# Performance work log

Measured on AMD Instinct MI355X. Metric: run time of the kernel, lower is better.

## Reference

```python
import jax, jax.numpy as jnp
import numpy as np

N_NODES = 100000
N_EDGES = 1600000
D_FEAT = 64
D_OUT = 64
K_HOPS = 2


def setup_inputs() -> dict:
    key = jax.random.key(0)
    k1, k2, k3, k4, k5 = jax.random.split(key, 5)
    feat = jax.random.normal(k1, (N_NODES, D_FEAT), dtype=jnp.float32)
    src = jax.random.randint(k2, (N_EDGES,), 0, N_NODES, dtype=jnp.int32)
    dst = jax.random.randint(k3, (N_EDGES,), 0, N_NODES, dtype=jnp.int32)
    # xavier-ish scale for fc1
    W1 = jax.random.normal(k4, (D_OUT, D_FEAT), dtype=jnp.float32) * (1.0 / np.sqrt(D_FEAT))
    b1 = jnp.zeros((D_OUT,), dtype=jnp.float32)
    return {"feat": feat, "src": src, "dst": dst, "W1": W1, "b1": b1}


def reference(feat, src, dst, W1, b1):
    # in-degrees (edges point src -> dst), clamp(min=1)
    deg = jax.ops.segment_sum(jnp.ones_like(dst, dtype=feat.dtype), dst,
                              num_segments=N_NODES)
    norm = jnp.power(jnp.maximum(deg, 1.0), -0.5)[:, None]  # [N, 1]
    # k hops of symmetric-normalized aggregation: h = D^-1/2 A D^-1/2 h
    for _ in range(K_HOPS):
        feat = feat * norm
        feat = jax.ops.segment_sum(feat[src], dst, num_segments=N_NODES)
        feat = feat * norm
    # fc1: x @ W1.T + b1
    return feat @ W1.T + b1
```

## Files before the change

kernel.cpp:

```cpp
#include <hip/hip_runtime.h>

#define NN 100000
#define NE 1600000
#define D 64
#define BSHIFT 7
#define NPB 128
#define NBUCK ((NN + NPB - 1) / NPB)
#define NCHUNK 512
#define CE (NE / NCHUNK)
#define CAP 4096
#define EBL 2560
#define NFC 1563

typedef unsigned int uint32;
typedef __attribute__((ext_vector_type(8))) short bf16x8;
typedef __attribute__((ext_vector_type(4))) float f32x4;

__device__ __forceinline__ uint32 f2bf(float f) {
    union { float f; uint32 i; } c; c.f = f;
    return (c.i + 0x7FFFu + ((c.i >> 16) & 1u)) >> 16;
}

__device__ __forceinline__ bf16x8 cvt8(const float* p) {
    float4 lo = *reinterpret_cast<const float4*>(p);
    float4 hi = *reinterpret_cast<const float4*>(p + 4);
    bf16x8 r;
    r[0] = (short)f2bf(lo.x); r[1] = (short)f2bf(lo.y);
    r[2] = (short)f2bf(lo.z); r[3] = (short)f2bf(lo.w);
    r[4] = (short)f2bf(hi.x); r[5] = (short)f2bf(hi.y);
    r[6] = (short)f2bf(hi.z); r[7] = (short)f2bf(hi.w);
    return r;
}

__global__ __launch_bounds__(256) void prep_part_kernel(const float* __restrict__ feat,
                                                        const float* __restrict__ W1,
                                                        unsigned short* __restrict__ fb,
                                                        const int* __restrict__ src,
                                                        const int* __restrict__ dst,
                                                        int* __restrict__ gcur,
                                                        int* __restrict__ ebuf) {
    __shared__ int ebl[CE];
    __shared__ unsigned short bkt[CE];
    __shared__ int cnt[NBUCK];
    __shared__ int bas[NBUCK];
    const int bid = blockIdx.x;
    if (bid >= NCHUNK) {
        const int wid = threadIdx.x >> 6;
        const int lane = threadIdx.x & 63;
        const int tile = (bid - NCHUNK) * 4 + wid;
        if (tile >= 6250) return;
        const int node0 = tile * 16;
        const int m = lane & 15;
        const int kg = lane >> 4;
        const float* frow = feat + (size_t)(node0 + m) * D + kg * 8;
        bf16x8 aF0 = cvt8(frow);
        bf16x8 aF1 = cvt8(frow + 32);
#pragma unroll
        for (int t = 0; t < 4; ++t) {
            const float* wrow = W1 + (size_t)(t * 16 + m) * D + kg * 8;
            bf16x8 bF0 = cvt8(wrow);
            bf16x8 bF1 = cvt8(wrow + 32);
            f32x4 acc = {0.f, 0.f, 0.f, 0.f};
            acc = __builtin_amdgcn_mfma_f32_16x16x32_bf16(aF0, bF0, acc, 0, 0, 0);
            acc = __builtin_amdgcn_mfma_f32_16x16x32_bf16(aF1, bF1, acc, 0, 0, 0);
            const int col = t * 16 + m;
#pragma unroll
            for (int r = 0; r < 4; ++r)
                fb[(size_t)(node0 + kg * 4 + r) * D + col] = (unsigned short)f2bf(acc[r]);
        }
        return;
    }
    for (int i = threadIdx.x; i < NBUCK; i += 256) cnt[i] = 0;
    __syncthreads();
    const int e0 = bid * CE;
    for (int i = threadIdx.x; i < CE; i += 256) {
        int d = dst[e0 + i], s = src[e0 + i];
        int b = d >> BSHIFT;
        ebl[i] = (s << BSHIFT) | (d & (NPB - 1));
        bkt[i] = (unsigned short)b;
        atomicAdd(&cnt[b], 1);
    }
    __syncthreads();
    for (int i = threadIdx.x; i < NBUCK; i += 256) {
        int c = cnt[i];
        bas[i] = c ? atomicAdd(&gcur[i], c) : 0;
    }
    __syncthreads();
    for (int i = threadIdx.x; i < NBUCK; i += 256) cnt[i] = 0;
    __syncthreads();
    for (int i = threadIdx.x; i < CE; i += 256) {
        int b = bkt[i];
        int p = bas[b] + atomicAdd(&cnt[b], 1);
        ebuf[(size_t)b * CAP + p] = ebl[i];
    }
}

__global__ __launch_bounds__(256) void bucketize_kernel(int* __restrict__ ebuf,
                                                        const int* __restrict__ gcur,
                                                        uint32* __restrict__ rpd,
                                                        float* __restrict__ norm) {
    __shared__ int ebl[EBL];
    __shared__ int cnt[NPB];
    __shared__ int sc[NPB + 1];
    __shared__ int lcur[NPB];
    const int b = blockIdx.x;
    const int base = b << BSHIFT;
    const int t = threadIdx.x;
    const int r0 = b * CAP;
    int len = gcur[b];
    if (len > EBL) len = EBL;
    if (t < NPB) { cnt[t] = 0; lcur[t] = 0; }
    if (t == 0) sc[0] = 0;
    __syncthreads();
    for (int e = t; e < len; e += 256) {
        int v = ebuf[r0 + e];
        ebl[e] = v;
        atomicAdd(&cnt[v & (NPB - 1)], 1);
    }
    __syncthreads();
    if (t < NPB) sc[t + 1] = cnt[t];
    __syncthreads();
    for (int off = 1; off < NPB; off <<= 1) {
        int v = (t < NPB && t >= off) ? sc[t + 1 - off] : 0;
        __syncthreads();
        if (t < NPB) sc[t + 1] += v;
        __syncthreads();
    }
    const int nval = min(NPB, NN - base);
    if (t < nval) {
        rpd[base + t] = ((uint32)(r0 + sc[t]) << 9) | (uint32)min(cnt[t], 511);
        norm[base + t] = rsqrtf(fmaxf((float)cnt[t], 1.0f));
    }
    __syncthreads();
    for (int e = t; e < len; e += 256) {
        int v = ebl[e];
        int ld = v & (NPB - 1);
        int p = r0 + sc[ld] + atomicAdd(&lcur[ld], 1);
        ebuf[p] = v & ~(NPB - 1);
    }
}

#define ACC8(Rr)                                 \
    a0 += __uint_as_float((Rr).x << 16);         \
    a1 += __uint_as_float((Rr).x & 0xFFFF0000u); \
    a2 += __uint_as_float((Rr).y << 16);         \
    a3 += __uint_as_float((Rr).y & 0xFFFF0000u); \
    a4 += __uint_as_float((Rr).z << 16);         \
    a5 += __uint_as_float((Rr).z & 0xFFFF0000u); \
    a6 += __uint_as_float((Rr).w << 16);         \
    a7 += __uint_as_float((Rr).w & 0xFFFF0000u);

#define ACC8W(Rr, W)                                   \
    a0 += (W) * __uint_as_float((Rr).x << 16);         \
    a1 += (W) * __uint_as_float((Rr).x & 0xFFFF0000u); \
    a2 += (W) * __uint_as_float((Rr).y << 16);         \
    a3 += (W) * __uint_as_float((Rr).y & 0xFFFF0000u); \
    a4 += (W) * __uint_as_float((Rr).z << 16);         \
    a5 += (W) * __uint_as_float((Rr).z & 0xFFFF0000u); \
    a6 += (W) * __uint_as_float((Rr).w << 16);         \
    a7 += (W) * __uint_as_float((Rr).w & 0xFFFF0000u);

#define STEP1(E)                                                           \
    {                                                                      \
        int o_ = csr[(E) + slot];                                          \
        uint4 r_ = *reinterpret_cast<const uint4*>(base + o_ + lo16);      \
        if constexpr (HOP == 1) { float w_ = norm[o_ >> 7]; ACC8W(r_, w_) } \
        else { ACC8(r_) }                                                  \
    }

template <int HOP>
__global__ __launch_bounds__(256) void gather_kernel(const unsigned short* __restrict__ in,
                                                     const uint32* __restrict__ rpd,
                                                     const int* __restrict__ csr,
                                                     const float* __restrict__ norm,
                                                     unsigned short* __restrict__ outb,
                                                     float* __restrict__ outf,
                                                     const float* __restrict__ b1) {
    const int node = blockIdx.x * 4 + (threadIdx.x >> 6);
    const int lane = threadIdx.x & 63;
    const int slot = lane >> 3;
    const int fo = (lane & 7) * 8;
    const int lo16 = (lane & 7) * 16;
    const char* base = (const char*)in;
    const uint32 v = rpd[node];
    int e = (int)(v >> 9);
    const int e1 = e + (int)(v & 511u);
    float a0 = 0, a1 = 0, a2 = 0, a3 = 0, a4 = 0, a5 = 0, a6 = 0, a7 = 0;
    for (; e + 16 <= e1; e += 16) {
        STEP1(e)
        STEP1(e + 8)
    }
    for (; e + 8 <= e1; e += 8) STEP1(e)
    if (e + slot < e1) STEP1(e)
#pragma unroll
    for (int off = 8; off <= 32; off <<= 1) {
        a0 += __shfl_xor(a0, off); a1 += __shfl_xor(a1, off);
        a2 += __shfl_xor(a2, off); a3 += __shfl_xor(a3, off);
        a4 += __shfl_xor(a4, off); a5 += __shfl_xor(a5, off);
        a6 += __shfl_xor(a6, off); a7 += __shfl_xor(a7, off);
    }
    if (slot == 0) {
        const float nd = norm[node];
        if (HOP == 1) {
            const float sc = nd * nd;
            uint4 o;
            o.x = f2bf(a0 * sc) | (f2bf(a1 * sc) << 16);
            o.y = f2bf(a2 * sc) | (f2bf(a3 * sc) << 16);
            o.z = f2bf(a4 * sc) | (f2bf(a5 * sc) << 16);
            o.w = f2bf(a6 * sc) | (f2bf(a7 * sc) << 16);
            *reinterpret_cast<uint4*>(outb + (size_t)node * D + fo) = o;
        } else {
            float4 bb = *reinterpret_cast<const float4*>(b1 + fo);
            float4 bc = *reinterpret_cast<const float4*>(b1 + fo + 4);
            float4 o1 = {a0 * nd + bb.x, a1 * nd + bb.y, a2 * nd + bb.z, a3 * nd + bb.w};
            float4 o2 = {a4 * nd + bc.x, a5 * nd + bc.y, a6 * nd + bc.z, a7 * nd + bc.w};
            float* op = outf + (size_t)node * D + fo;
            *reinterpret_cast<float4*>(op) = o1;
            *reinterpret_cast<float4*>(op + 4) = o2;
        }
    }
}

extern "C" void kernel_launch(void* const* d_in, const int* in_sizes, int n_in,
                              void* d_out, int out_size, void* d_ws, size_t ws_size,
                              hipStream_t stream) {
    const float* feat = (const float*)d_in[0];
    const int* src    = (const int*)d_in[1];
    const int* dst    = (const int*)d_in[2];
    const float* W1   = (const float*)d_in[3];
    const float* b1   = (const float*)d_in[4];
    float* out        = (float*)d_out;

    uint32*         rpd  = (uint32*)d_ws;
    float*          norm = (float*)(rpd + NN);
    int*            gcur = (int*)(norm + NN);
    int*            csr  = gcur + 1024;
    unsigned short* t1b  = (unsigned short*)(csr + (size_t)NBUCK * CAP);
    unsigned short* fb   = (unsigned short*)d_out;

    hipMemsetAsync(gcur, 0, NBUCK * sizeof(int), stream);
    prep_part_kernel<<<NCHUNK + NFC, 256, 0, stream>>>(feat, W1, fb, src, dst, gcur, csr);
    bucketize_kernel<<<NBUCK, 256, 0, stream>>>(csr, gcur, rpd, norm);

    gather_kernel<1><<<NN / 4, 256, 0, stream>>>(fb, rpd, csr, norm, t1b, nullptr, nullptr);
    gather_kernel<2><<<NN / 4, 256, 0, stream>>>(t1b, rpd, csr, norm, nullptr, out, b1);
}
```

Before: 144.0 us.

## Replace global atomic bucket offsets with per-chunk prefix tables and local partitioning

Each edge chunk now scans its own bucket counts and writes the edges locally sorted by bucket within its chunk slice, plus a per-chunk offset table. This removes the global atomicAdd on bucket cursors and the memset. The bucketize kernel reads each chunk's segment for its bucket via a prefix over chunks and builds the CSR in a separate buffer with a smaller per-bucket capacity. In exchange it reads 512 small scattered segments per bucket with a serial per-thread copy loop, and it aliases t1b onto ebuf.

```diff
diff --git a/kernel.cpp b/kernel.cpp
--- a/kernel.cpp
+++ b/kernel.cpp
@@ -8,8 +8,8 @@
 #define NBUCK ((NN + NPB - 1) / NPB)
 #define NCHUNK 512
 #define CE (NE / NCHUNK)
-#define CAP 4096
-#define EBL 2560
+#define BSTR (NBUCK + 1)
+#define CAPC 2560
 #define NFC 1563
 
 typedef unsigned int uint32;
@@ -32,21 +32,23 @@
     return r;
 }
 
-__global__ __launch_bounds__(256) void prep_part_kernel(const float* __restrict__ feat,
-                                                        const float* __restrict__ W1,
-                                                        unsigned short* __restrict__ fb,
-                                                        const int* __restrict__ src,
-                                                        const int* __restrict__ dst,
-                                                        int* __restrict__ gcur,
-                                                        int* __restrict__ ebuf) {
+__global__ __launch_bounds__(256) void build_kernel(const float* __restrict__ feat,
+                                                    const float* __restrict__ W1,
+                                                    unsigned short* __restrict__ fb,
+                                                    const int* __restrict__ src,
+                                                    const int* __restrict__ dst,
+                                                    int* __restrict__ basG,
+                                                    int* __restrict__ ebuf) {
     __shared__ int ebl[CE];
     __shared__ unsigned short bkt[CE];
     __shared__ int cnt[NBUCK];
-    __shared__ int bas[NBUCK];
+    __shared__ int sc[NBUCK + 1];
+    __shared__ int tsum[256];
     const int bid = blockIdx.x;
+    const int t = threadIdx.x;
     if (bid >= NCHUNK) {
-        const int wid = threadIdx.x >> 6;
-        const int lane = threadIdx.x & 63;
+        const int wid = t >> 6;
+        const int lane = t & 63;
         const int tile = (bid - NCHUNK) * 4 + wid;
         if (tile >= 6250) return;
         const int node0 = tile * 16;
@@ -56,24 +58,24 @@
         bf16x8 aF0 = cvt8(frow);
         bf16x8 aF1 = cvt8(frow + 32);
 #pragma unroll
-        for (int t = 0; t < 4; ++t) {
-            const float* wrow = W1 + (size_t)(t * 16 + m) * D + kg * 8;
+        for (int tt = 0; tt < 4; ++tt) {
+            const float* wrow = W1 + (size_t)(tt * 16 + m) * D + kg * 8;
             bf16x8 bF0 = cvt8(wrow);
             bf16x8 bF1 = cvt8(wrow + 32);
             f32x4 acc = {0.f, 0.f, 0.f, 0.f};
             acc = __builtin_amdgcn_mfma_f32_16x16x32_bf16(aF0, bF0, acc, 0, 0, 0);
             acc = __builtin_amdgcn_mfma_f32_16x16x32_bf16(aF1, bF1, acc, 0, 0, 0);
-            const int col = t * 16 + m;
+            const int col = tt * 16 + m;
 #pragma unroll
             for (int r = 0; r < 4; ++r)
                 fb[(size_t)(node0 + kg * 4 + r) * D + col] = (unsigned short)f2bf(acc[r]);
         }
         return;
     }
-    for (int i = threadIdx.x; i < NBUCK; i += 256) cnt[i] = 0;
+    for (int i = t; i < NBUCK; i += 256) cnt[i] = 0;
     __syncthreads();
     const int e0 = bid * CE;
-    for (int i = threadIdx.x; i < CE; i += 256) {
+    for (int i = t; i < CE; i += 256) {
         int d = dst[e0 + i], s = src[e0 + i];
         int b = d >> BSHIFT;
         ebl[i] = (s << BSHIFT) | (d & (NPB - 1));
@@ -81,62 +83,112 @@
         atomicAdd(&cnt[b], 1);
     }
     __syncthreads();
-    for (int i = threadIdx.x; i < NBUCK; i += 256) {
-        int c = cnt[i];
-        bas[i] = c ? atomicAdd(&gcur[i], c) : 0;
-    }
-    __syncthreads();
-    for (int i = threadIdx.x; i < NBUCK; i += 256) cnt[i] = 0;
-    __syncthreads();
-    for (int i = threadIdx.x; i < CE; i += 256) {
+    const int j0 = t * 4;
+    int v0 = (j0 + 0 < NBUCK) ? cnt[j0 + 0] : 0;
+    int v1 = (j0 + 1 < NBUCK) ? cnt[j0 + 1] : 0;
+    int v2 = (j0 + 2 < NBUCK) ? cnt[j0 + 2] : 0;
+    int v3 = (j0 + 3 < NBUCK) ? cnt[j0 + 3] : 0;
+    int s0 = v0, s1 = s0 + v1, s2 = s1 + v2, s3 = s2 + v3;
+    tsum[t] = s3;
+    __syncthreads();
+    for (int off = 1; off < 256; off <<= 1) {
+        int y = (t >= off) ? tsum[t - off] : 0;
+        __syncthreads();
+        tsum[t] += y;
+        __syncthreads();
+    }
+    const int pre = (t > 0) ? tsum[t - 1] : 0;
+    if (j0 + 0 < NBUCK) sc[j0 + 0] = pre;
+    if (j0 + 1 < NBUCK) sc[j0 + 1] = pre + s0;
+    if (j0 + 2 < NBUCK) sc[j0 + 2] = pre + s1;
+    if (j0 + 3 < NBUCK) sc[j0 + 3] = pre + s2;
+    if (t == 0) sc[NBUCK] = CE;
+    __syncthreads();
+    int* brow = basG + (size_t)bid * BSTR;
+    for (int j = t; j < BSTR; j += 256) brow[j] = sc[j];
+    for (int i = t; i < NBUCK; i += 256) cnt[i] = 0;
+    __syncthreads();
+    for (int i = t; i < CE; i += 256) {
         int b = bkt[i];
-        int p = bas[b] + atomicAdd(&cnt[b], 1);
-        ebuf[(size_t)b * CAP + p] = ebl[i];
-    }
-}
-
-__global__ __launch_bounds__(256) void bucketize_kernel(int* __restrict__ ebuf,
-                                                        const int* __restrict__ gcur,
+        int p = sc[b] + atomicAdd(&cnt[b], 1);
+        ebuf[e0 + p] = ebl[i];
+    }
+}
+
+__global__ __launch_bounds__(256) void bucketize_kernel(const int* __restrict__ ebuf,
+                                                        const int* __restrict__ basG,
+                                                        int* __restrict__ csr,
                                                         uint32* __restrict__ rpd,
                                                         float* __restrict__ norm) {
-    __shared__ int ebl[EBL];
+    __shared__ int stage[CAPC];
+    __shared__ int clo[NCHUNK];
+    __shared__ int clen[NCHUNK];
+    __shared__ int cpre[NCHUNK + 1];
+    __shared__ int tsum[256];
     __shared__ int cnt[NPB];
-    __shared__ int sc[NPB + 1];
+    __shared__ int sc2[NPB + 1];
     __shared__ int lcur[NPB];
     const int b = blockIdx.x;
     const int base = b << BSHIFT;
     const int t = threadIdx.x;
-    const int r0 = b * CAP;
-    int len = gcur[b];
-    if (len > EBL) len = EBL;
+    for (int c = t; c < NCHUNK; c += 256) {
+        int lo = basG[(size_t)c * BSTR + b];
+        int hi = basG[(size_t)c * BSTR + b + 1];
+        clo[c] = lo;
+        clen[c] = hi - lo;
+    }
     if (t < NPB) { cnt[t] = 0; lcur[t] = 0; }
-    if (t == 0) sc[0] = 0;
-    __syncthreads();
-    for (int e = t; e < len; e += 256) {
-        int v = ebuf[r0 + e];
-        ebl[e] = v;
-        atomicAdd(&cnt[v & (NPB - 1)], 1);
-    }
-    __syncthreads();
-    if (t < NPB) sc[t + 1] = cnt[t];
+    if (t == 0) sc2[0] = 0;
+    __syncthreads();
+    const int c0 = t * 2;
+    int w0 = clen[c0], w1 = clen[c0 + 1];
+    int u0 = w0, u1 = u0 + w1;
+    tsum[t] = u1;
+    __syncthreads();
+    for (int off = 1; off < 256; off <<= 1) {
+        int y = (t >= off) ? tsum[t - off] : 0;
+        __syncthreads();
+        tsum[t] += y;
+        __syncthreads();
+    }
+    const int pre = (t > 0) ? tsum[t - 1] : 0;
+    cpre[c0] = pre;
+    cpre[c0 + 1] = pre + u0;
+    if (t == 255) cpre[NCHUNK] = tsum[255];
+    __syncthreads();
+    int total = cpre[NCHUNK];
+    if (total > CAPC) total = CAPC;
+    for (int c = t; c < NCHUNK; c += 256) {
+        int lo = clo[c];
+        int n = clen[c];
+        int p = cpre[c];
+        if (p + n > CAPC) n = (p < CAPC) ? (CAPC - p) : 0;
+        const int* seg = ebuf + (size_t)c * CE + lo;
+        for (int k = 0; k < n; ++k) stage[p + k] = seg[k];
+    }
+    __syncthreads();
+    for (int e = t; e < total; e += 256)
+        atomicAdd(&cnt[stage[e] & (NPB - 1)], 1);
+    __syncthreads();
+    if (t < NPB) sc2[t + 1] = cnt[t];
     __syncthreads();
     for (int off = 1; off < NPB; off <<= 1) {
-        int v = (t < NPB && t >= off) ? sc[t + 1 - off] : 0;
-        __syncthreads();
-        if (t < NPB) sc[t + 1] += v;
+        int v = (t < NPB && t >= off) ? sc2[t + 1 - off] : 0;
+        __syncthreads();
+        if (t < NPB) sc2[t + 1] += v;
         __syncthreads();
     }
     const int nval = min(NPB, NN - base);
     if (t < nval) {
-        rpd[base + t] = ((uint32)(r0 + sc[t]) << 9) | (uint32)min(cnt[t], 511);
+        rpd[base + t] = ((uint32)(b * CAPC + sc2[t]) << 9) | (uint32)min(cnt[t], 511);
         norm[base + t] = rsqrtf(fmaxf((float)cnt[t], 1.0f));
     }
     __syncthreads();
-    for (int e = t; e < len; e += 256) {
-        int v = ebl[e];
+    for (int e = t; e < total; e += 256) {
+        int v = stage[e];
         int ld = v & (NPB - 1);
-        int p = r0 + sc[ld] + atomicAdd(&lcur[ld], 1);
-        ebuf[p] = v & ~(NPB - 1);
+        int p = b * CAPC + sc2[ld] + atomicAdd(&lcur[ld], 1);
+        csr[p] = v & ~(NPB - 1);
     }
 }
 
@@ -233,14 +285,14 @@
 
     uint32*         rpd  = (uint32*)d_ws;
     float*          norm = (float*)(rpd + NN);
-    int*            gcur = (int*)(norm + NN);
-    int*            csr  = gcur + 1024;
-    unsigned short* t1b  = (unsigned short*)(csr + (size_t)NBUCK * CAP);
+    int*            basG = (int*)(norm + NN);
+    int*            csr  = basG + (size_t)NCHUNK * BSTR;
+    int*            ebuf = csr + (size_t)NBUCK * CAPC;
+    unsigned short* t1b  = (unsigned short*)ebuf;
     unsigned short* fb   = (unsigned short*)d_out;
 
-    hipMemsetAsync(gcur, 0, NBUCK * sizeof(int), stream);
-    prep_part_kernel<<<NCHUNK + NFC, 256, 0, stream>>>(feat, W1, fb, src, dst, gcur, csr);
-    bucketize_kernel<<<NBUCK, 256, 0, stream>>>(csr, gcur, rpd, norm);
+    build_kernel<<<NCHUNK + NFC, 256, 0, stream>>>(feat, W1, fb, src, dst, basG, ebuf);
+    bucketize_kernel<<<NBUCK, 256, 0, stream>>>(ebuf, basG, csr, rpd, norm);
 
     gather_kernel<1><<<NN / 4, 256, 0, stream>>>(fb, rpd, csr, norm, t1b, nullptr, nullptr);
     gather_kernel<2><<<NN / 4, 256, 0, stream>>>(t1b, rpd, csr, norm, nullptr, out, b1);
```

Result: faster. 133.2 us (-7.4%).
